# Kernel optimization log

Hardware: AMD Instinct MI355X
Metric: run time of the kernel (lower is better)

## Reference

```python
import jax, jax.numpy as jnp
import numpy as np

K = 4
IN_PLANES = 256
OUT_PLANES = 256
KSIZE = 3
HIDDEN = int(IN_PLANES * 0.25) + 1  # 65, per attention2d (in_planes != 3)
TEMPERATURE = 34.0
STRIDE = 1
PAD = 1


def setup_inputs() -> dict:
    key = jax.random.key(0)
    k1, k2, k3, k4, k5 = jax.random.split(key, 5)
    x = jax.random.normal(k1, (16, IN_PLANES, 64, 64), dtype=jnp.float32)
    # Dynamic kernel bank: (K, out, in//groups, k, k), kaiming-like scale
    fan = IN_PLANES * KSIZE * KSIZE
    weight = jax.random.normal(k2, (K, OUT_PLANES, IN_PLANES, KSIZE, KSIZE), dtype=jnp.float32) * np.float32(np.sqrt(2.0 / fan))
    # attention 1x1 convs act on pooled [B,C] vectors -> plain matmuls
    att_w1 = jax.random.normal(k3, (HIDDEN, IN_PLANES), dtype=jnp.float32) * 0.05  # conv1 (no bias)
    att_w2 = jax.random.normal(k4, (K, HIDDEN), dtype=jnp.float32) * 0.05          # conv2 weight
    att_b2 = jax.random.normal(k5, (K,), dtype=jnp.float32) * 0.05                 # conv2 bias
    return {"x": x, "weight": weight, "att_w1": att_w1, "att_w2": att_w2, "att_b2": att_b2}


def _forward(x, weight, att_w1, att_w2, att_b2):
    # attention2d: global avg pool -> 1x1 conv -> relu -> 1x1 conv -> softmax(. / T)
    pooled = x.mean(axis=(2, 3))                          # [B, C]
    h = jax.nn.relu(pooled @ att_w1.T)                    # [B, hidden]
    logits = h @ att_w2.T + att_b2                        # [B, K]
    att = jax.nn.softmax(logits / TEMPERATURE, axis=-1)   # [B, K]

    # per-sample aggregated kernels: [B, out, in, k, k]
    agg_w = jnp.einsum('bk,koihw->boihw', att, weight)

    # groups = batch_size conv == vmap of a normal conv with per-sample weight
    def conv_one(xi, wi):
        return jax.lax.conv_general_dilated(
            xi[None], wi,
            window_strides=(STRIDE, STRIDE),
            padding=((PAD, PAD), (PAD, PAD)),
            dimension_numbers=('NCHW', 'OIHW', 'NCHW'))[0]

    out = jax.vmap(conv_one)(x, agg_w)                    # [B, out, H, W]
    # NOTE: original forward computes norm+activation but returns the raw conv
    # output, so they are intentionally omitted here.
    return out


def reference(x, weight, att_w1, att_w2, att_b2):
    return _forward(x, weight, att_w1, att_w2, att_b2)
```

## Files before the change

### kernel.cpp

```cpp
#include <hip/hip_runtime.h>
#include <hip/hip_bf16.h>
#include <stdint.h>

#define B_ 16
#define C_ 256
#define O_ 256
#define H_ 64
#define W_ 64
#define HP 66
#define WP 66
#define HIDDEN 65
#define TEMP 34.0f
#define BK 32
#define LDK 40

typedef __bf16 bf16x8 __attribute__((ext_vector_type(8)));
typedef float floatx16 __attribute__((ext_vector_type(16)));
typedef unsigned int uint;
typedef unsigned short ushort;

__device__ __forceinline__ ushort f2bf(float f) {
    union { float f; uint32_t u; } v; v.f = f;
    uint32_t u = v.u;
    uint32_t r = (u + 0x7FFFu + ((u >> 16) & 1u)) >> 16;
    return (ushort)r;
}

#define LTR 132
__global__ __launch_bounds__(256) void pad_pool_kernel(
    const float* __restrict__ x, ushort* __restrict__ xp,
    float* __restrict__ pooled)
{
    int b  = blockIdx.x / HP;
    int hp = blockIdx.x % HP;
    ushort* xpb = xp + ((size_t)(b * HP + hp)) * WP * C_;
    int tid = threadIdx.x;

    if (hp == 0 || hp == HP - 1) {
        uint* p = (uint*)xpb;
        for (int i = tid; i < WP * C_ / 2; i += 256) p[i] = 0;
        return;
    }
    int h = hp - 1;

    __shared__ uint  tr[64 * LTR];
    __shared__ float pr[8 * 256];

    int wq = tid & 15;
    int sw = (wq & 3) << 3;
    const float* xb = x + (((size_t)b * C_) * H_ + h) * W_ + wq * 4;
    #pragma unroll
    for (int i = 0; i < 8; i++) {
        int cp = i * 16 + (tid >> 4);
        const float* p0 = xb + (size_t)(2 * cp) * H_ * W_;
        float4 v0 = *(const float4*)p0;
        float4 v1 = *(const float4*)(p0 + H_ * W_);
        uint r0 = (uint)f2bf(v0.x) | ((uint)f2bf(v1.x) << 16);
        uint r1 = (uint)f2bf(v0.y) | ((uint)f2bf(v1.y) << 16);
        uint r2 = (uint)f2bf(v0.z) | ((uint)f2bf(v1.z) << 16);
        uint r3 = (uint)f2bf(v0.w) | ((uint)f2bf(v1.w) << 16);
        int col = cp ^ sw;
        tr[(wq * 4 + 0) * LTR + col] = r0;
        tr[(wq * 4 + 1) * LTR + col] = r1;
        tr[(wq * 4 + 2) * LTR + col] = r2;
        tr[(wq * 4 + 3) * LTR + col] = r3;
    }

    if (tid < 32) {
        *(uint4*)(xpb + tid * 8) = uint4{0, 0, 0, 0};
    } else if (tid < 64) {
        *(uint4*)(xpb + (size_t)65 * C_ + (tid - 32) * 8) = uint4{0, 0, 0, 0};
    }
    __syncthreads();

    int cg = tid & 31;
    int wg = tid >> 5;
    float acc[8] = {0, 0, 0, 0, 0, 0, 0, 0};
    #pragma unroll
    for (int i = 0; i < 8; i++) {
        int w = i * 8 + wg;
        int s = ((w >> 2) & 3) << 3;
        uint4 d = *(const uint4*)(&tr[w * LTR + ((cg * 4) ^ s)]);
        *(uint4*)(xpb + (size_t)(w + 1) * C_ + cg * 8) = d;
        acc[0] += __uint_as_float(d.x << 16);
        acc[1] += __uint_as_float(d.x & 0xffff0000u);
        acc[2] += __uint_as_float(d.y << 16);
        acc[3] += __uint_as_float(d.y & 0xffff0000u);
        acc[4] += __uint_as_float(d.z << 16);
        acc[5] += __uint_as_float(d.z & 0xffff0000u);
        acc[6] += __uint_as_float(d.w << 16);
        acc[7] += __uint_as_float(d.w & 0xffff0000u);
    }
    #pragma unroll
    for (int k = 0; k < 8; k++) pr[wg * 256 + cg * 8 + k] = acc[k];
    __syncthreads();

    float s = 0.f;
    #pragma unroll
    for (int j = 0; j < 8; j++) s += pr[j * 256 + tid];
    atomicAdd(&pooled[b * C_ + tid], s);
}

__global__ __launch_bounds__(256) void att_agg_kernel(
    const float* __restrict__ weight, const float* __restrict__ pooled,
    const float* __restrict__ w1, const float* __restrict__ w2,
    const float* __restrict__ b2, ushort* __restrict__ aggw)
{
    int o = blockIdx.x;
    int tid = threadIdx.x;
    __shared__ float psh[B_ * C_];
    __shared__ float hsh[B_ * HIDDEN];
    __shared__ float a_sh[64];

    for (int i = tid; i < B_ * C_; i += 256) psh[i] = pooled[i] * (1.0f / (H_ * W_));
    __syncthreads();
    for (int i = tid; i < B_ * HIDDEN; i += 256) {
        int bb = i / HIDDEN, j = i % HIDDEN;
        float s = 0.f;
        for (int c = 0; c < C_; c++) s += psh[bb * C_ + c] * w1[j * C_ + c];
        hsh[i] = fmaxf(s, 0.f);
    }
    __syncthreads();
    if (tid < B_) {
        float lg[4];
        float mx = -1e30f;
        for (int k = 0; k < 4; k++) {
            float s = b2[k];
            for (int j = 0; j < HIDDEN; j++) s += hsh[tid * HIDDEN + j] * w2[k * HIDDEN + j];
            lg[k] = s / TEMP;
            mx = fmaxf(mx, lg[k]);
        }
        float den = 0.f;
        for (int k = 0; k < 4; k++) { lg[k] = expf(lg[k] - mx); den += lg[k]; }
        for (int k = 0; k < 4; k++) a_sh[tid * 4 + k] = lg[k] / den;
    }
    __syncthreads();

    int cp = tid & 127, bh = tid >> 7;
    float wv[4][18];
    #pragma unroll
    for (int k = 0; k < 4; k++) {
        const float* wp_ = weight + (((size_t)k * O_ + o) * C_ + cp * 2) * 9;
        #pragma unroll
        for (int t = 0; t < 18; t++) wv[k][t] = wp_[t];
    }
    uint* dst = (uint*)aggw;
    for (int b = bh * 8; b < bh * 8 + 8; b++) {
        float a0 = a_sh[b * 4 + 0], a1 = a_sh[b * 4 + 1];
        float a2 = a_sh[b * 4 + 2], a3 = a_sh[b * 4 + 3];
        #pragma unroll
        for (int t = 0; t < 9; t++) {
            float s0 = a0 * wv[0][t]     + a1 * wv[1][t]     + a2 * wv[2][t]     + a3 * wv[3][t];
            float s1 = a0 * wv[0][9 + t] + a1 * wv[1][9 + t] + a2 * wv[2][9 + t] + a3 * wv[3][9 + t];
            uint p = (uint)f2bf(s0) | ((uint)f2bf(s1) << 16);
            dst[(((size_t)b * 9 + t) * O_ + o) * (C_ / 2) + cp] = p;
        }
    }
}

__global__ __launch_bounds__(256, 2) void conv_kernel(
    const ushort* __restrict__ xp,
    const ushort* __restrict__ aggw,
    float* __restrict__ out)
{
    __shared__ ushort As[3 * 128 * LDK];
    __shared__ ushort Bs[264 * LDK];

    int bid = blockIdx.x;
    int xcd = bid & 7, slot = bid >> 3;
    int pair = xcd * 4 + (slot >> 4);
    int nt = slot & 15;
    int b = pair >> 1, mt = pair & 1;

    int tid = threadIdx.x;
    int r0 = nt * 4;

    int wave = tid >> 6, lane = tid & 63;
    int wm = wave >> 1, wn = wave & 1;
    int n31 = lane & 31, h = lane >> 5;

    int Ag[6], Al[6];
    #pragma unroll
    for (int s = 0; s < 6; s++) {
        int cid = tid + 256 * s;
        int kc = cid & 3, row = (cid >> 2) & 127, tt = cid >> 9;
        Ag[s] = (tt * O_ + row) * C_ + kc * 8;
        Al[s] = (tt * 128 + row) * LDK + kc * 8;
    }
    int Bg[5], Bl[5];
    #pragma unroll
    for (int s = 0; s < 5; s++) {
        int cid = tid + 256 * s;
        int kc = cid & 3, rw = cid >> 2;
        int wr_ = rw / 66, wp = rw - wr_ * 66;
        Bg[s] = ((r0 + wr_) * WP + wp) * C_ + kc * 8;
        Bl[s] = rw * LDK + kc * 8;
    }
    const ushort* gA0 = aggw + ((size_t)b * 9 * O_ + (size_t)mt * 128) * C_;
    const ushort* gB0 = xp + (size_t)b * HP * WP * C_;

    int aO[2];
    #pragma unroll
    for (int im = 0; im < 2; im++)
        aO[im] = (wm * 64 + im * 32 + n31) * LDK + h * 8;
    int bO[3][4];
    #pragma unroll
    for (int tx = 0; tx < 3; tx++)
        #pragma unroll
        for (int jn = 0; jn < 4; jn++) {
            int nb = wn * 128 + jn * 32;
            bO[tx][jn] = ((nb >> 6) * 66 + (nb & 63) + tx + n31) * LDK + h * 8;
        }

    floatx16 acc[2][4] = {};

    for (int ty = 0; ty < 3; ty++) {
        const ushort* gA = gA0 + (size_t)(ty * 3) * O_ * C_;
        const ushort* gB = gB0 + (size_t)ty * WP * C_;
        for (int c0 = 0; c0 < C_; c0 += BK) {
            __syncthreads();
            #pragma unroll
            for (int s = 0; s < 6; s++)
                *(uint4*)(&As[Al[s]]) = *(const uint4*)(gA + Ag[s] + c0);
            #pragma unroll
            for (int s = 0; s < 4; s++)
                *(uint4*)(&Bs[Bl[s]]) = *(const uint4*)(gB + Bg[s] + c0);
            if (tid < 32)
                *(uint4*)(&Bs[Bl[4]]) = *(const uint4*)(gB + Bg[4] + c0);
            __syncthreads();

            #pragma unroll
            for (int tx = 0; tx < 3; tx++) {
                #pragma unroll
                for (int ks = 0; ks < 2; ks++) {
                    int ko = ks * 16;
                    bf16x8 af0 = *(const bf16x8*)(&As[tx * 128 * LDK + aO[0] + ko]);
                    bf16x8 af1 = *(const bf16x8*)(&As[tx * 128 * LDK + aO[1] + ko]);
                    bf16x8 bf[4];
                    #pragma unroll
                    for (int jn = 0; jn < 4; jn++)
                        bf[jn] = *(const bf16x8*)(&Bs[bO[tx][jn] + ko]);
                    #pragma unroll
                    for (int jn = 0; jn < 4; jn++)
                        acc[0][jn] = __builtin_amdgcn_mfma_f32_32x32x16_bf16(af0, bf[jn], acc[0][jn], 0, 0, 0);
                    #pragma unroll
                    for (int jn = 0; jn < 4; jn++)
                        acc[1][jn] = __builtin_amdgcn_mfma_f32_32x32x16_bf16(af1, bf[jn], acc[1][jn], 0, 0, 0);
                }
            }
        }
    }

    float* outb = out + ((size_t)b * O_ + (size_t)mt * 128) * (H_ * W_) + (size_t)nt * 256;
    #pragma unroll
    for (int im = 0; im < 2; im++) {
        int obase = wm * 64 + im * 32 + 4 * h;
        #pragma unroll
        for (int jn = 0; jn < 4; jn++) {
            int pcol = wn * 128 + jn * 32 + n31;
            #pragma unroll
            for (int g = 0; g < 4; g++)
                #pragma unroll
                for (int r4 = 0; r4 < 4; r4++)
                    outb[(size_t)(obase + r4 + 8 * g) * (H_ * W_) + pcol] = acc[im][jn][g * 4 + r4];
        }
    }
}

extern "C" void kernel_launch(void* const* d_in, const int* in_sizes, int n_in,
                              void* d_out, int out_size, void* d_ws, size_t ws_size,
                              hipStream_t stream) {
    const float* x      = (const float*)d_in[0];
    const float* weight = (const float*)d_in[1];
    const float* att_w1 = (const float*)d_in[2];
    const float* att_w2 = (const float*)d_in[3];
    const float* att_b2 = (const float*)d_in[4];
    float* out = (float*)d_out;

    char* ws = (char*)d_ws;
    float* pooled  = (float*)ws;
    ushort* aggw   = (ushort*)(ws + 32768);
    ushort* xp     = (ushort*)(ws + 32768 + 18874368);

    hipMemsetAsync(pooled, 0, B_ * C_ * sizeof(float), stream);
    pad_pool_kernel<<<B_ * HP, 256, 0, stream>>>(x, xp, pooled);
    att_agg_kernel<<<O_, 256, 0, stream>>>(weight, pooled, att_w1, att_w2, att_b2, aggw);
    conv_kernel<<<512, 256, 0, stream>>>(xp, aggw, out);
}
```

Baseline: 238.3 us.

## Double-buffer conv tiles with direct global-to-LDS loads and XOR swizzle

Rewrites the conv GEMM main loop so each 512-thread block covers all 256 output channels. Operand tiles are loaded straight into LDS with global_load_lds and double-buffered, so the next K-slice streams in while MFMAs run on the current one. A padded LDS stride is replaced by an XOR swizzle to avoid bank conflicts, and s_setprio is raised during compute. This cuts the grid to 256 blocks and doubles LDS use per block, which may limit occupancy. It also depends on hand-placed vmcnt waits being correct.

```diff
diff --git a/kernel.cpp b/kernel.cpp
--- a/kernel.cpp
+++ b/kernel.cpp
@@ -12,7 +12,6 @@
 #define HIDDEN 65
 #define TEMP 34.0f
 #define BK 32
-#define LDK 40
 
 typedef __bf16 bf16x8 __attribute__((ext_vector_type(8)));
 typedef float floatx16 __attribute__((ext_vector_type(16)));
@@ -158,100 +157,144 @@
     }
 }
 
-__global__ __launch_bounds__(256, 2) void conv_kernel(
+__device__ __forceinline__ void gl_lds16(const ushort* g, ushort* l) {
+    __builtin_amdgcn_global_load_lds(
+        (__attribute__((address_space(1))) void*)(uintptr_t)g,
+        (__attribute__((address_space(3))) void*)l,
+        16, 0, 0);
+}
+
+__global__ __launch_bounds__(512, 2) void conv_kernel(
     const ushort* __restrict__ xp,
     const ushort* __restrict__ aggw,
     float* __restrict__ out)
 {
-    __shared__ ushort As[3 * 128 * LDK];
-    __shared__ ushort Bs[264 * LDK];
+    __shared__ ushort As[2][3 * 256 * 32];
+    __shared__ ushort Bs[2][272 * 32];
 
     int bid = blockIdx.x;
-    int xcd = bid & 7, slot = bid >> 3;
-    int pair = xcd * 4 + (slot >> 4);
-    int nt = slot & 15;
-    int b = pair >> 1, mt = pair & 1;
+    int xcd = bid & 7, sl8 = bid >> 3;
+    int b  = xcd * 2 + (sl8 >> 4);
+    int nt = sl8 & 15;
+    int r0 = nt * 4;
 
     int tid = threadIdx.x;
-    int r0 = nt * 4;
-
     int wave = tid >> 6, lane = tid & 63;
     int wm = wave >> 1, wn = wave & 1;
     int n31 = lane & 31, h = lane >> 5;
 
-    int Ag[6], Al[6];
-    #pragma unroll
-    for (int s = 0; s < 6; s++) {
-        int cid = tid + 256 * s;
-        int kc = cid & 3, row = (cid >> 2) & 127, tt = cid >> 9;
-        Ag[s] = (tt * O_ + row) * C_ + kc * 8;
-        Al[s] = (tt * 128 + row) * LDK + kc * 8;
-    }
-    int Bg[5], Bl[5];
-    #pragma unroll
-    for (int s = 0; s < 5; s++) {
-        int cid = tid + 256 * s;
-        int kc = cid & 3, rw = cid >> 2;
+    const ushort* gA0 = aggw + (size_t)b * 9 * O_ * C_;
+    const ushort* gB0 = xp + (size_t)b * HP * WP * C_;
+
+    int gAoff[6];
+    #pragma unroll
+    for (int j = 0; j < 6; j++) {
+        int i = j * 512 + tid;
+        int tt = i >> 10, rem = i & 1023;
+        int row = rem >> 2, p = rem & 3;
+        int sw = p ^ ((row >> 1) & 3);
+        gAoff[j] = (tt * O_ + row) * C_ + sw * 8;
+    }
+    int gBoff[2], gBoffT;
+    #pragma unroll
+    for (int j = 0; j < 2; j++) {
+        int i = j * 512 + tid;
+        int rw = i >> 2, p = i & 3;
+        int sw = p ^ ((rw >> 1) & 3);
         int wr_ = rw / 66, wp = rw - wr_ * 66;
-        Bg[s] = ((r0 + wr_) * WP + wp) * C_ + kc * 8;
-        Bl[s] = rw * LDK + kc * 8;
-    }
-    const ushort* gA0 = aggw + ((size_t)b * 9 * O_ + (size_t)mt * 128) * C_;
-    const ushort* gB0 = xp + (size_t)b * HP * WP * C_;
-
-    int aO[2];
-    #pragma unroll
-    for (int im = 0; im < 2; im++)
-        aO[im] = (wm * 64 + im * 32 + n31) * LDK + h * 8;
-    int bO[3][4];
+        gBoff[j] = ((r0 + wr_) * WP + wp) * C_ + sw * 8;
+    }
+    {
+        int i = 1024 + lane;
+        int rw = i >> 2, p = i & 3;
+        int sw = p ^ ((rw >> 1) & 3);
+        int wr_ = rw / 66, wp = rw - wr_ * 66;
+        gBoffT = ((r0 + wr_) * WP + wp) * C_ + sw * 8;
+    }
+
+    int aOff[2];
+    #pragma unroll
+    for (int im = 0; im < 2; im++) {
+        int row = wm * 64 + im * 32 + n31;
+        aOff[im] = row * 32 + ((h ^ ((row >> 1) & 3)) << 3);
+    }
+    int bOff[3][4];
     #pragma unroll
     for (int tx = 0; tx < 3; tx++)
         #pragma unroll
         for (int jn = 0; jn < 4; jn++) {
             int nb = wn * 128 + jn * 32;
-            bO[tx][jn] = ((nb >> 6) * 66 + (nb & 63) + tx + n31) * LDK + h * 8;
+            int rw = (nb >> 6) * 66 + (nb & 63) + tx + n31;
+            bOff[tx][jn] = rw * 32 + ((h ^ ((rw >> 1) & 3)) << 3);
         }
 
     floatx16 acc[2][4] = {};
 
-    for (int ty = 0; ty < 3; ty++) {
-        const ushort* gA = gA0 + (size_t)(ty * 3) * O_ * C_;
-        const ushort* gB = gB0 + (size_t)ty * WP * C_;
-        for (int c0 = 0; c0 < C_; c0 += BK) {
-            __syncthreads();
+    ushort* A0 = &As[0][0]; ushort* A1 = &As[1][0];
+    ushort* B0 = &Bs[0][0]; ushort* B1 = &Bs[1][0];
+
+    auto ISSUE = [&](int t, ushort* Aw, ushort* Bw) {
+        int tyn = t >> 3, cn = (t & 7) * BK;
+        const ushort* gA = gA0 + (size_t)(tyn * 3) * O_ * C_ + cn;
+        const ushort* gB = gB0 + (size_t)tyn * WP * C_ + cn;
+        #pragma unroll
+        for (int j = 0; j < 6; j++)
+            gl_lds16(gA + gAoff[j], Aw + (j * 8 + wave) * 512);
+        #pragma unroll
+        for (int j = 0; j < 2; j++)
+            gl_lds16(gB + gBoff[j], Bw + (j * 8 + wave) * 512);
+        if (wave == 0 && lane < 32)
+            gl_lds16(gB + gBoffT, Bw + 16 * 512);
+    };
+
+    auto COMPUTE = [&](const ushort* Aq, const ushort* Bq) {
+        __builtin_amdgcn_s_setprio(1);
+        #pragma unroll
+        for (int tx = 0; tx < 3; tx++) {
             #pragma unroll
-            for (int s = 0; s < 6; s++)
-                *(uint4*)(&As[Al[s]]) = *(const uint4*)(gA + Ag[s] + c0);
-            #pragma unroll
-            for (int s = 0; s < 4; s++)
-                *(uint4*)(&Bs[Bl[s]]) = *(const uint4*)(gB + Bg[s] + c0);
-            if (tid < 32)
-                *(uint4*)(&Bs[Bl[4]]) = *(const uint4*)(gB + Bg[4] + c0);
-            __syncthreads();
-
-            #pragma unroll
-            for (int tx = 0; tx < 3; tx++) {
+            for (int ks = 0; ks < 2; ks++) {
+                const int kx = ks << 4;
+                bf16x8 af0 = *(const bf16x8*)(Aq + tx * 8192 + (aOff[0] ^ kx));
+                bf16x8 af1 = *(const bf16x8*)(Aq + tx * 8192 + (aOff[1] ^ kx));
+                bf16x8 bv[4];
                 #pragma unroll
-                for (int ks = 0; ks < 2; ks++) {
-                    int ko = ks * 16;
-                    bf16x8 af0 = *(const bf16x8*)(&As[tx * 128 * LDK + aO[0] + ko]);
-                    bf16x8 af1 = *(const bf16x8*)(&As[tx * 128 * LDK + aO[1] + ko]);
-                    bf16x8 bf[4];
-                    #pragma unroll
-                    for (int jn = 0; jn < 4; jn++)
-                        bf[jn] = *(const bf16x8*)(&Bs[bO[tx][jn] + ko]);
-                    #pragma unroll
-                    for (int jn = 0; jn < 4; jn++)
-                        acc[0][jn] = __builtin_amdgcn_mfma_f32_32x32x16_bf16(af0, bf[jn], acc[0][jn], 0, 0, 0);
-                    #pragma unroll
-                    for (int jn = 0; jn < 4; jn++)
-                        acc[1][jn] = __builtin_amdgcn_mfma_f32_32x32x16_bf16(af1, bf[jn], acc[1][jn], 0, 0, 0);
-                }
+                for (int jn = 0; jn < 4; jn++)
+                    bv[jn] = *(const bf16x8*)(Bq + (bOff[tx][jn] ^ kx));
+                #pragma unroll
+                for (int jn = 0; jn < 4; jn++)
+                    acc[0][jn] = __builtin_amdgcn_mfma_f32_32x32x16_bf16(af0, bv[jn], acc[0][jn], 0, 0, 0);
+                #pragma unroll
+                for (int jn = 0; jn < 4; jn++)
+                    acc[1][jn] = __builtin_amdgcn_mfma_f32_32x32x16_bf16(af1, bv[jn], acc[1][jn], 0, 0, 0);
             }
         }
-    }
-
-    float* outb = out + ((size_t)b * O_ + (size_t)mt * 128) * (H_ * W_) + (size_t)nt * 256;
+        __builtin_amdgcn_s_setprio(0);
+    };
+
+    ISSUE(0, A0, B0);
+    ISSUE(1, A1, B1);
+
+    for (int s = 0; s < 22; s += 2) {
+        asm volatile("s_waitcnt vmcnt(8)" ::: "memory");
+        __builtin_amdgcn_s_barrier();
+        COMPUTE(A0, B0);
+        __builtin_amdgcn_s_barrier();
+        ISSUE(s + 2, A0, B0);
+
+        asm volatile("s_waitcnt vmcnt(8)" ::: "memory");
+        __builtin_amdgcn_s_barrier();
+        COMPUTE(A1, B1);
+        __builtin_amdgcn_s_barrier();
+        ISSUE(s + 3, A1, B1);
+    }
+    asm volatile("s_waitcnt vmcnt(8)" ::: "memory");
+    __builtin_amdgcn_s_barrier();
+    COMPUTE(A0, B0);
+    asm volatile("s_waitcnt vmcnt(0)" ::: "memory");
+    __builtin_amdgcn_s_barrier();
+    COMPUTE(A1, B1);
+
+    float* outb = out + (size_t)b * O_ * (H_ * W_) + (size_t)nt * 256;
     #pragma unroll
     for (int im = 0; im < 2; im++) {
         int obase = wm * 64 + im * 32 + 4 * h;
@@ -285,5 +328,5 @@
     hipMemsetAsync(pooled, 0, B_ * C_ * sizeof(float), stream);
     pad_pool_kernel<<<B_ * HP, 256, 0, stream>>>(x, xp, pooled);
     att_agg_kernel<<<O_, 256, 0, stream>>>(weight, pooled, att_w1, att_w2, att_b2, aggw);
-    conv_kernel<<<512, 256, 0, stream>>>(xp, aggw, out);
-}
+    conv_kernel<<<256, 512, 0, stream>>>(xp, aggw, out);
+}
```

Measured after the change: 238.9 us. About the same (+0.3%).
